# Performance work log

Measured on AMD Instinct MI355X. Metric: run time of the kernel, lower is better.

## Reference

```python
import jax, jax.numpy as jnp
import numpy as np

TAU = 0.25            # leaky-integrator time constant
OUTPUT_TICKS = 4      # inference output_ticks
T, B, P, H, S, C = 20, 16384, 256, 512, 512, 128  # timesteps, batch, pho, hidden_ps, sem, sem_cleanup


def setup_inputs() -> dict:
    key = jax.random.key(0)
    ks = jax.random.split(key, 9)
    u = lambda k, shape: jax.random.uniform(k, shape, jnp.float32, -0.1, 0.1)
    return {
        "inputs": jax.random.normal(ks[0], (T, B, P), jnp.float32),
        "w_hps_ph": u(ks[1], (P, H)),
        "w_hps_hs": u(ks[2], (H, S)),
        "w_ss": u(ks[3], (S, S)),
        "w_sc": u(ks[4], (S, C)),
        "w_cs": u(ks[5], (C, S)),
        "bias_hps": u(ks[6], (H,)),
        "bias_s": u(ks[7], (S,)),
        "bias_css": u(ks[8], (C,)),
    }


def reference(inputs, w_hps_ph, w_hps_hs, w_ss, w_sc, w_cs, bias_hps, bias_s, bias_css):
    """HS04 task_pho_sem, inference mode (no weight noise).
    Leaky-integrator recurrence over timesteps; returns sigmoid semantic
    activations for the last OUTPUT_TICKS steps: (OUTPUT_TICKS, B, S)."""
    n_t, b, _ = inputs.shape
    h = w_hps_ph.shape[1]
    s_dim = w_ss.shape[0]
    c_dim = w_cs.shape[0]
    sig = jax.nn.sigmoid
    one_m_tau = 1.0 - TAU

    init = (
        jnp.zeros((b, h), jnp.float32),   # input_hps
        jnp.zeros((b, s_dim), jnp.float32),  # input_s
        jnp.zeros((b, c_dim), jnp.float32),  # input_css
        jnp.full((b, h), 0.5, jnp.float32),  # act_hps
        jnp.full((b, s_dim), 0.5, jnp.float32),  # act_s
        jnp.full((b, c_dim), 0.5, jnp.float32),  # act_css
    )

    def step(carry, x_t):
        in_hps, in_s, in_css, a_hps, a_s, a_css = carry
        hps = TAU * (x_t @ w_hps_ph + bias_hps) + one_m_tau * in_hps
        s = TAU * (a_hps @ w_hps_hs + a_s @ w_ss + a_css @ w_cs + bias_s) + one_m_tau * in_s
        css = TAU * (a_s @ w_sc + bias_css) + one_m_tau * in_css
        a_s_new = sig(s)
        new_carry = (hps, s, css, sig(hps), a_s_new, sig(css))
        return new_carry, a_s_new

    _, act_s_all = jax.lax.scan(step, init, inputs)  # (T, B, S)
    return act_s_all[-OUTPUT_TICKS:]
```

## Files before the change

kernel.cpp:

```cpp
#include <hip/hip_runtime.h>

#define TAU 0.25f
#define OMT 0.75f

typedef __attribute__((ext_vector_type(8))) short  bfrag8;
typedef __attribute__((ext_vector_type(4))) float  f4acc;
typedef __attribute__((ext_vector_type(4))) float  fvec4;
typedef __attribute__((ext_vector_type(2))) unsigned uvec2;
typedef __attribute__((ext_vector_type(4))) unsigned uvec4;

#define WS_PACKH 0u
#define WS_PACKS 262144u
#define WS_PACKC 1441792u
#define WS_BIAS  1572864u

__device__ __forceinline__ unsigned short f2bf(float f) {
    unsigned u = __builtin_bit_cast(unsigned, f);
    u = (u + 0x7FFFu + ((u >> 16) & 1u)) >> 16;
    return (unsigned short)u;
}

__global__ void hs04_prep(const float* __restrict__ wph, const float* __restrict__ whs,
                          const float* __restrict__ wss, const float* __restrict__ wsc,
                          const float* __restrict__ wcs, const float* __restrict__ bh,
                          const float* __restrict__ bs,  const float* __restrict__ bc,
                          unsigned char* __restrict__ ws)
{
    int gid = blockIdx.x * 256 + threadIdx.x;
    if (gid < 98304) {
        int lane = gid & 63, frag = gid >> 6;
        int cls, nt, ks; size_t off;
        if (frag < 256)       { cls = 0; nt = frag >> 3;       ks = frag & 7;
                                off = WS_PACKH + (size_t)nt*8192  + (size_t)ks*1024; }
        else if (frag < 1408) { int f = frag - 256;  cls = 1; nt = f / 36; ks = f - nt*36;
                                off = WS_PACKS + (size_t)nt*36864 + (size_t)ks*1024; }
        else                  { int f = frag - 1408; cls = 2; nt = f >> 4; ks = f & 15;
                                off = WS_PACKC + (size_t)nt*16384 + (size_t)ks*1024; }
        int q = lane >> 4, rr = lane & 15;
        unsigned short v[8];
        #pragma unroll
        for (int j = 0; j < 8; ++j) {
            int k = ks*32 + q*8 + j;
            int n = nt*16 + rr;
            float wv;
            if (cls == 0)      wv = wph[k*512 + n];
            else if (cls == 1) wv = (k < 512)  ? whs[k*512 + n]
                               : (k < 1024) ? wss[(k-512)*512 + n]
                                            : wcs[(k-1024)*512 + n];
            else               wv = wsc[k*128 + n];
            v[j] = f2bf(wv);
        }
        uvec4 pk = { (unsigned)v[0] | ((unsigned)v[1] << 16),
                     (unsigned)v[2] | ((unsigned)v[3] << 16),
                     (unsigned)v[4] | ((unsigned)v[5] << 16),
                     (unsigned)v[6] | ((unsigned)v[7] << 16) };
        *(uvec4*)(ws + off + (size_t)lane*16) = pk;
    } else if (gid < 98304 + 1152) {
        int col = gid - 98304;
        float b = (col < 512) ? bh[col] : (col < 1024 ? bs[col-512] : bc[col-1024]);
        ((float*)(ws + WS_BIAS))[col] = TAU * b;
    }
}

__global__ __launch_bounds__(512, 2) void hs04_main(const float* __restrict__ x_all,
                                                    const unsigned char* __restrict__ ws,
                                                    float* __restrict__ out)
{
    extern __shared__ char smem[];
    char* const acts = smem;
    char* const xbuf = smem + 147456;

    const int tid  = threadIdx.x;
    const int lane = tid & 63;
    const int wu   = __builtin_amdgcn_readfirstlane(tid >> 6);
    const int q    = lane >> 4;
    const int r    = lane & 15;
    const int b0   = blockIdx.x << 6;

    {
        unsigned hv = f2bf(0.125f);
        unsigned u  = hv | (hv << 16);
        uvec4 fill = {u, u, u, u};
        uvec4* p = (uvec4*)acts;
        for (int i = tid; i < 9216; i += 512) p[i] = fill;
    }

    float tb[9];
    {
        const float* bias = (const float*)(ws + WS_BIAS);
        #pragma unroll
        for (int j = 0; j < 9; ++j) {
            int cb = (j < 4) ? wu*64 + j*16 : (j < 8) ? 512 + wu*64 + (j-4)*16 : 1024 + wu*16;
            tb[j] = bias[cb + r];
        }
    }

    f4acc acc[9][4];
    #pragma unroll
    for (int j = 0; j < 9; ++j) {
        float tbj = tb[j];
        #pragma unroll
        for (int m = 0; m < 4; ++m) acc[j][m] = {tbj, tbj, tbj, tbj};
    }

    const bfrag8* bHp[4]; const bfrag8* bSp[4]; const bfrag8* bCp;
    #pragma unroll
    for (int j = 0; j < 4; ++j) {
        bHp[j] = (const bfrag8*)(ws + WS_PACKH + (size_t)(wu*4+j)*8192)  + lane;
        bSp[j] = (const bfrag8*)(ws + WS_PACKS + (size_t)(wu*4+j)*36864) + lane;
    }
    bCp = (const bfrag8*)(ws + WS_PACKC + (size_t)wu*16384) + lane;

    auto stageX_load = [&](const float* xt, int mt, fvec4 (&v)[2]) {
        const fvec4* src = (const fvec4*)xt + (size_t)mt*1024;
        v[0] = __builtin_nontemporal_load(src + tid);
        v[1] = __builtin_nontemporal_load(src + tid + 512);
    };
    auto stageX_write = [&](const fvec4 (&v)[2], char* dst) {
        #pragma unroll
        for (int i = 0; i < 2; ++i) {
            int f4i = tid + i*512;
            int row = f4i >> 6, c4 = f4i & 63;
            unsigned lo = (unsigned)f2bf(TAU*v[i].x) | ((unsigned)f2bf(TAU*v[i].y) << 16);
            unsigned hi = (unsigned)f2bf(TAU*v[i].z) | ((unsigned)f2bf(TAU*v[i].w) << 16);
            uvec2 d = {lo, hi};
            *(uvec2*)(dst + row*512 + (((c4 >> 1) ^ row) << 4) + ((c4 & 1) << 3)) = d;
        }
    };
    auto loadBS = [&](int ks, bfrag8 (&d)[4]) {
        #pragma unroll
        for (int j = 0; j < 4; ++j) d[j] = bSp[j][ks*64];
    };
    auto loadA2 = [&](int ks, bfrag8 (&d)[4]) {
        const char* p = acts + r*2304 + ((((ks << 2) + q) ^ r) << 4);
        #pragma unroll
        for (int m = 0; m < 4; ++m) d[m] = *(const bfrag8*)(p + m*36864);
    };
    auto mm16 = [&](bfrag8 (&a)[4], bfrag8 (&b)[4]) {
        #pragma unroll
        for (int j = 0; j < 4; ++j)
            #pragma unroll
            for (int m = 0; m < 4; ++m)
                acc[4+j][m] = __builtin_amdgcn_mfma_f32_16x16x32_bf16(a[m], b[j], acc[4+j][m], 0, 0, 0);
    };
    auto mmc = [&](bfrag8 (&a)[4], bfrag8 c) {
        #pragma unroll
        for (int m = 0; m < 4; ++m)
            acc[8][m] = __builtin_amdgcn_mfma_f32_16x16x32_bf16(a[m], c, acc[8][m], 0, 0, 0);
    };

    {
        fvec4 xv0[2];
        stageX_load(x_all + (size_t)b0*256, 0, xv0);
        stageX_write(xv0, xbuf);
    }
    __syncthreads();

    for (int t = 0; t < 20; ++t) {
        const float* xt = x_all + ((size_t)t*16384 + (size_t)b0)*256;
        fvec4 xv[2];

        #pragma unroll
        for (int mt = 0; mt < 4; ++mt) {
            if (mt < 3) stageX_load(xt, mt+1, xv);
            const char* xb = xbuf + (mt & 1)*8192;
            bfrag8 hb0[4], hb1[4];
            #pragma unroll
            for (int j = 0; j < 4; ++j) hb0[j] = bHp[j][0];
            #pragma unroll 1
            for (int k2 = 0; k2 < 8; k2 += 2) {
                #pragma unroll
                for (int j = 0; j < 4; ++j) hb1[j] = bHp[j][(k2+1)*64];
                {
                    bfrag8 ha = *(const bfrag8*)(xb + r*512 + ((((k2 << 2) + q) ^ r) << 4));
                    #pragma unroll
                    for (int j = 0; j < 4; ++j)
                        acc[j][mt] = __builtin_amdgcn_mfma_f32_16x16x32_bf16(ha, hb0[j], acc[j][mt], 0, 0, 0);
                }
                if (k2 + 2 < 8) {
                    #pragma unroll
                    for (int j = 0; j < 4; ++j) hb0[j] = bHp[j][(k2+2)*64];
                }
                {
                    bfrag8 ha = *(const bfrag8*)(xb + r*512 + (((((k2+1) << 2) + q) ^ r) << 4));
                    #pragma unroll
                    for (int j = 0; j < 4; ++j)
                        acc[j][mt] = __builtin_amdgcn_mfma_f32_16x16x32_bf16(ha, hb1[j], acc[j][mt], 0, 0, 0);
                }
            }
            if (mt < 3) {
                stageX_write(xv, xbuf + ((mt+1) & 1)*8192);
                __syncthreads();
            }
        }

        {
            bfrag8 sa0[4], sa1[4], sb0[4], sb1[4];
            loadBS(0, sb0); loadA2(0, sa0);
            #pragma unroll 1
            for (int ks = 0; ks < 16; ks += 2) {
                loadBS(ks+1, sb1); loadA2(ks+1, sa1);
                mm16(sa0, sb0);
                loadBS(ks+2, sb0); loadA2(ks+2, sa0);
                mm16(sa1, sb1);
            }
            #pragma unroll 1
            for (int ks = 16; ks < 32; ks += 2) {
                bfrag8 c0 = bCp[(ks-16)*64];
                loadBS(ks+1, sb1); loadA2(ks+1, sa1);
                mm16(sa0, sb0);
                mmc(sa0, c0);
                bfrag8 c1 = bCp[(ks-15)*64];
                loadBS(ks+2, sb0); loadA2(ks+2, sa0);
                mm16(sa1, sb1);
                mmc(sa1, c1);
            }
            if (t < 19) stageX_load(xt + 16384*256, 0, xv);
            #pragma unroll 1
            for (int ks = 32; ks < 36; ks += 2) {
                loadBS(ks+1, sb1); loadA2(ks+1, sa1);
                mm16(sa0, sb0);
                if (ks + 2 < 36) { loadBS(ks+2, sb0); loadA2(ks+2, sa0); }
                mm16(sa1, sb1);
            }
            if (t < 19) stageX_write(xv, xbuf);
        }

        __syncthreads();
        {
            const bool emit = (t >= 16);
            #pragma unroll
            for (int j = 0; j < 9; ++j) {
                int cb = (j < 4) ? wu*64 + j*16 : (j < 8) ? 512 + wu*64 + (j-4)*16 : 1024 + wu*16;
                int col   = cb + r;
                int chunk = col >> 3;
                int coff  = (col & 7) << 1;
                float tbj = tb[j];
                #pragma unroll
                for (int m = 0; m < 4; ++m) {
                    f4acc v = acc[j][m];
                    #pragma unroll
                    for (int e = 0; e < 4; ++e) {
                        int rl  = q*4 + e;
                        int row = m*16 + rl;
                        float in = v[e];
                        float a  = 1.0f / (1.0f + __expf(-in));
                        *(unsigned short*)(acts + row*2304 + ((chunk ^ rl) << 4) + coff) = f2bf(TAU * a);
                        if (emit && j >= 4 && j < 8) {
                            __builtin_nontemporal_store(
                                a, out + ((size_t)(t-16)*16384 + (size_t)(b0 + row))*512 + (col - 512));
                        }
                    }
                    acc[j][m] = v*OMT + tbj;
                }
            }
        }
        __syncthreads();
    }
}

extern "C" void kernel_launch(void* const* d_in, const int* in_sizes, int n_in,
                              void* d_out, int out_size, void* d_ws, size_t ws_size,
                              hipStream_t stream) {
    const float* x   = (const float*)d_in[0];
    const float* wph = (const float*)d_in[1];
    const float* whs = (const float*)d_in[2];
    const float* wss = (const float*)d_in[3];
    const float* wsc = (const float*)d_in[4];
    const float* wcs = (const float*)d_in[5];
    const float* bh  = (const float*)d_in[6];
    const float* bs  = (const float*)d_in[7];
    const float* bc  = (const float*)d_in[8];
    unsigned char* ws = (unsigned char*)d_ws;
    float* outp = (float*)d_out;

    hipFuncSetAttribute((const void*)hs04_main,
                        hipFuncAttributeMaxDynamicSharedMemorySize, 163840);

    hipLaunchKernelGGL(hs04_prep, dim3(389), dim3(256), 0, stream,
                       wph, whs, wss, wsc, wcs, bh, bs, bc, ws);
    hipLaunchKernelGGL(hs04_main, dim3(256), dim3(512), 163840, stream,
                       x, ws, outp);
}
```

Baseline: 2.118 ms.

## Hoist Hp weight fragments, deepen S-phase prefetch pipeline, drop trailing barrier

The hidden-phase weight fragments are now loaded once per timestep into registers and reused across all four M-tiles, instead of being reloaded inside each tile. The semantic GEMM loop moves from double- to quad-buffered fragment prefetch, with the tail written out explicitly. The end-of-timestep barrier is removed, since later barriers in the next step appear to already order the activation reuse. This cuts redundant LDS traffic and sync stalls, but adds a large register load that could cause spills or lower occupancy.

```diff
diff --git a/kernel.cpp b/kernel.cpp
--- a/kernel.cpp
+++ b/kernel.cpp
@@ -157,36 +157,25 @@
     __syncthreads();
 
     for (int t = 0; t < 20; ++t) {
-        const float* xt = x_all + ((size_t)t*16384 + (size_t)b0)*256;
+        const float* xt = x_all + ((size_t)t*16384 + (size_t)b0) * 256;
         fvec4 xv[2];
+
+        bfrag8 hB[8][4];
+        #pragma unroll
+        for (int ks = 0; ks < 8; ++ks)
+            #pragma unroll
+            for (int j = 0; j < 4; ++j) hB[ks][j] = bHp[j][ks*64];
 
         #pragma unroll
         for (int mt = 0; mt < 4; ++mt) {
             if (mt < 3) stageX_load(xt, mt+1, xv);
             const char* xb = xbuf + (mt & 1)*8192;
-            bfrag8 hb0[4], hb1[4];
-            #pragma unroll
-            for (int j = 0; j < 4; ++j) hb0[j] = bHp[j][0];
-            #pragma unroll 1
-            for (int k2 = 0; k2 < 8; k2 += 2) {
+            #pragma unroll
+            for (int ks = 0; ks < 8; ++ks) {
+                bfrag8 ha = *(const bfrag8*)(xb + r*512 + ((((ks << 2) + q) ^ r) << 4));
                 #pragma unroll
-                for (int j = 0; j < 4; ++j) hb1[j] = bHp[j][(k2+1)*64];
-                {
-                    bfrag8 ha = *(const bfrag8*)(xb + r*512 + ((((k2 << 2) + q) ^ r) << 4));
-                    #pragma unroll
-                    for (int j = 0; j < 4; ++j)
-                        acc[j][mt] = __builtin_amdgcn_mfma_f32_16x16x32_bf16(ha, hb0[j], acc[j][mt], 0, 0, 0);
-                }
-                if (k2 + 2 < 8) {
-                    #pragma unroll
-                    for (int j = 0; j < 4; ++j) hb0[j] = bHp[j][(k2+2)*64];
-                }
-                {
-                    bfrag8 ha = *(const bfrag8*)(xb + r*512 + (((((k2+1) << 2) + q) ^ r) << 4));
-                    #pragma unroll
-                    for (int j = 0; j < 4; ++j)
-                        acc[j][mt] = __builtin_amdgcn_mfma_f32_16x16x32_bf16(ha, hb1[j], acc[j][mt], 0, 0, 0);
-                }
+                for (int j = 0; j < 4; ++j)
+                    acc[j][mt] = __builtin_amdgcn_mfma_f32_16x16x32_bf16(ha, hB[ks][j], acc[j][mt], 0, 0, 0);
             }
             if (mt < 3) {
                 stageX_write(xv, xbuf + ((mt+1) & 1)*8192);
@@ -195,38 +184,36 @@
         }
 
         {
-            bfrag8 sa0[4], sa1[4], sb0[4], sb1[4];
-            loadBS(0, sb0); loadA2(0, sa0);
+            bfrag8 sbA[4], sbB[4], sbC[4], sbD[4];
+            bfrag8 saA[4], saB[4], saC[4], saD[4];
+            loadBS(0, sbA); loadBS(1, sbB); loadBS(2, sbC);
+            loadA2(0, saA); loadA2(1, saB);
             #pragma unroll 1
-            for (int ks = 0; ks < 16; ks += 2) {
-                loadBS(ks+1, sb1); loadA2(ks+1, sa1);
-                mm16(sa0, sb0);
-                loadBS(ks+2, sb0); loadA2(ks+2, sa0);
-                mm16(sa1, sb1);
+            for (int ksb = 0; ksb < 16; ksb += 4) {
+                loadBS(ksb+3, sbD); loadA2(ksb+2, saC); mm16(saA, sbA);
+                loadBS(ksb+4, sbA); loadA2(ksb+3, saD); mm16(saB, sbB);
+                loadBS(ksb+5, sbB); loadA2(ksb+4, saA); mm16(saC, sbC);
+                loadBS(ksb+6, sbC); loadA2(ksb+5, saB); mm16(saD, sbD);
             }
             #pragma unroll 1
-            for (int ks = 16; ks < 32; ks += 2) {
-                bfrag8 c0 = bCp[(ks-16)*64];
-                loadBS(ks+1, sb1); loadA2(ks+1, sa1);
-                mm16(sa0, sb0);
-                mmc(sa0, c0);
-                bfrag8 c1 = bCp[(ks-15)*64];
-                loadBS(ks+2, sb0); loadA2(ks+2, sa0);
-                mm16(sa1, sb1);
-                mmc(sa1, c1);
+            for (int ksb = 16; ksb < 32; ksb += 4) {
+                bfrag8 c0 = bCp[(ksb-16)*64], c1 = bCp[(ksb-15)*64];
+                bfrag8 c2 = bCp[(ksb-14)*64], c3 = bCp[(ksb-13)*64];
+                loadBS(ksb+3, sbD); loadA2(ksb+2, saC); mm16(saA, sbA); mmc(saA, c0);
+                loadBS(ksb+4, sbA); loadA2(ksb+3, saD); mm16(saB, sbB); mmc(saB, c1);
+                loadBS(ksb+5, sbB); loadA2(ksb+4, saA); mm16(saC, sbC); mmc(saC, c2);
+                loadBS(ksb+6, sbC); loadA2(ksb+5, saB); mm16(saD, sbD); mmc(saD, c3);
             }
             if (t < 19) stageX_load(xt + 16384*256, 0, xv);
-            #pragma unroll 1
-            for (int ks = 32; ks < 36; ks += 2) {
-                loadBS(ks+1, sb1); loadA2(ks+1, sa1);
-                mm16(sa0, sb0);
-                if (ks + 2 < 36) { loadBS(ks+2, sb0); loadA2(ks+2, sa0); }
-                mm16(sa1, sb1);
-            }
+            loadBS(35, sbD); loadA2(34, saC); mm16(saA, sbA);
+            loadA2(35, saD);                  mm16(saB, sbB);
+            mm16(saC, sbC);
+            mm16(saD, sbD);
             if (t < 19) stageX_write(xv, xbuf);
         }
 
         __syncthreads();
+
         {
             const bool emit = (t >= 16);
             #pragma unroll
@@ -255,7 +242,6 @@
                 }
             }
         }
-        __syncthreads();
     }
 }
 
```

Result: slower. 2.548 ms (+20.3%).
